# Performance work log

Hardware: AMD Instinct MI355X
Metric: run time of the kernel (lower is better)

## Reference

```python
import jax, jax.numpy as jnp
import numpy as np

B, C, H, W = 8, 256, 128, 128
KC, VC, HEADS = 256, 256, 8


def setup_inputs() -> dict:
    key = jax.random.key(0)
    ks = jax.random.split(key, 10)
    s = 0.05
    return {
        "x": jax.random.normal(ks[0], (B, C, H, W), jnp.float32),
        "Wk": jax.random.normal(ks[1], (KC, C), jnp.float32) * s,
        "bk": jax.random.normal(ks[2], (KC,), jnp.float32) * s,
        "Wq": jax.random.normal(ks[3], (KC, C), jnp.float32) * s,
        "bq": jax.random.normal(ks[4], (KC,), jnp.float32) * s,
        "Wv": jax.random.normal(ks[5], (VC, C), jnp.float32) * s,
        "bv": jax.random.normal(ks[6], (VC,), jnp.float32) * s,
        "Wr": jax.random.normal(ks[7], (C, VC), jnp.float32) * s,
        "br": jax.random.normal(ks[8], (C,), jnp.float32) * s,
        "head_count": HEADS,
    }


def reference(x, Wk, bk, Wq, bq, Wv, bv, Wr, br, head_count):
    n, c, h, w = x.shape
    hw = h * w
    xf = x.reshape(n, c, hw)  # [n, C, S]
    # 1x1 convs == per-pixel linear projections
    keys = jnp.einsum('kc,ncs->nks', Wk, xf) + bk[None, :, None]
    queries = jnp.einsum('kc,ncs->nks', Wq, xf) + bq[None, :, None]
    values = jnp.einsum('vc,ncs->nvs', Wv, xf) + bv[None, :, None]

    dk = Wk.shape[0] // head_count
    dv = Wv.shape[0] // head_count
    # split heads along channel dim (matches torch channel slicing)
    K = jax.nn.softmax(keys.reshape(n, head_count, dk, hw), axis=-1)   # softmax over spatial
    Q = jax.nn.softmax(queries.reshape(n, head_count, dk, hw), axis=2) # softmax over key dim
    V = values.reshape(n, head_count, dv, hw)

    # context = K @ V^T : [n, h, dk, dv]
    ctx = jnp.einsum('nhks,nhvs->nhkv', K, V)
    # attended = ctx^T @ Q : [n, h, dv, S]
    att = jnp.einsum('nhkv,nhks->nhvs', ctx, Q).reshape(n, head_count * dv, h, w)

    attention = jnp.einsum('ov,nvhw->nohw', Wr, att) + br[None, :, None, None]
    # attention map: per-head mean over key dim, then mean over heads
    attention_map = K.mean(axis=2).mean(axis=1).reshape(n, h, w)
    # torch returns the LAST head's context (loop variable after the loop)
    context_last = ctx[:, -1]
    return attention, context_last, attention_map
```

## Files before the change

### kernel.cpp

```cpp
#include <hip/hip_runtime.h>
#include <hip/hip_bf16.h>

typedef float f32x4 __attribute__((ext_vector_type(4)));
typedef short s16x8 __attribute__((ext_vector_type(8)));
typedef short s16x4 __attribute__((ext_vector_type(4)));
typedef __bf16 bf16x8 __attribute__((ext_vector_type(8)));
typedef unsigned short u16;

#define DEVI __device__ __forceinline__

static constexpr int    HW      = 16384;
static constexpr size_t BSTRIDE = (size_t)256 * HW;

static constexpr size_t oXBT   = 0;
static constexpr size_t oEK    = oXBT  + (size_t)8 * HW * 256 * 2;
static constexpr size_t oQT    = oEK   + (size_t)8 * 256 * HW * 2;
static constexpr size_t oVB    = oQT   + (size_t)8 * HW * 256 * 2;
static constexpr size_t oWK    = oVB   + (size_t)8 * 256 * HW * 2;
static constexpr size_t oBIAS  = oWK   + (size_t)768 * 256 * 2;
static constexpr size_t oISE   = oBIAS + 4096;
static constexpr size_t oPS    = oISE  + 8192;
static constexpr size_t oCTX   = oPS   + (size_t)256 * 2048 * 4;
static constexpr size_t oMB    = oCTX  + (size_t)64 * 1024 * 4;
static constexpr size_t oCPART = oMB   + (size_t)8 * 256 * 256 * 2;
static constexpr size_t oMPART = oCPART + (size_t)4096 * 1024 * 4;

DEVI float bf2f(short x) {
  unsigned u = ((unsigned)(unsigned short)x) << 16;
  return __builtin_bit_cast(float, u);
}
DEVI u16 f2bf(float x) { return __builtin_bit_cast(u16, (__bf16)x); }

DEVI void gld16(const void* g, void* l) {
  __builtin_amdgcn_global_load_lds(
      (__attribute__((address_space(1))) void*)(g),
      (__attribute__((address_space(3))) void*)(l), 16, 0, 0);
}

__global__ __launch_bounds__(256) void k_prep(
    const float* __restrict__ Wk, const float* __restrict__ Wq, const float* __restrict__ Wv,
    const float* __restrict__ bk, const float* __restrict__ bq, const float* __restrict__ bv,
    u16* __restrict__ Wkqv, float* __restrict__ bias)
{
  int i = blockIdx.x * 256 + threadIdx.x;
  for (int p = i; p < 768 * 256; p += 64 * 256) {
    float v = (p < 65536) ? Wk[p] : (p < 131072 ? Wq[p - 65536] : Wv[p - 131072]);
    Wkqv[p] = f2bf(v);
  }
  if (i < 768) bias[i] = (i < 256) ? bk[i] : (i < 512 ? bq[i - 256] : bv[i - 512]);
}

__global__ __launch_bounds__(256) void k_transpose(const float* __restrict__ in_, u16* __restrict__ out)
{
  __shared__ u16 lds[64 * 256];
  const int t = threadIdx.x;
  const int n = blockIdx.y;
  const int s0 = blockIdx.x * 64;
  const float* src = in_ + ((size_t)n * 256 + t) * HW + s0;
  #pragma unroll
  for (int i = 0; i < 16; ++i) {
    f32x4 v = *(const f32x4*)(src + i * 4);
    #pragma unroll
    for (int j = 0; j < 4; ++j) lds[(i * 4 + j) * 256 + t] = f2bf(v[j]);
  }
  __syncthreads();
  s16x8* gp = (s16x8*)(out + (size_t)n * BSTRIDE + (size_t)s0 * 256);
  const s16x8* lp = (const s16x8*)lds;
  #pragma unroll
  for (int i = 0; i < 8; ++i) gp[t + i * 256] = lp[t + i * 256];
}


#define GEMM_CORE(Ab, Bb)                                                                   \
  u16* Al = smem;                                                                           \
  u16* Bl = smem + 16384;                                                                   \
  auto STAGE = [&](int buf, int kt) {                                                       \
    const int k0 = kt * 64;                                                                 \
    _Pragma("unroll")                                                                       \
    for (int i = 0; i < 4; ++i) {                                                           \
      const int r_ = i * 32 + (t >> 3);                                                     \
      const int cs = (((t & 7) ^ (r_ & 7)) * 8);                                            \
      gld16((Ab) + (size_t)r_ * 256 + k0 + cs, Al + buf * 8192 + i * 2048 + t * 8);         \
      gld16((Bb) + (size_t)r_ * 256 + k0 + cs, Bl + buf * 8192 + i * 2048 + t * 8);         \
    }                                                                                       \
  };                                                                                        \
  f32x4 acc[4][4] = {};                                                                     \
  STAGE(0, 0); STAGE(1, 1);                                                                 \
  _Pragma("unroll")                                                                         \
  for (int kt = 0; kt < 4; ++kt) {                                                          \
    if (kt < 3) asm volatile("s_waitcnt vmcnt(8)" ::: "memory");                            \
    else        asm volatile("s_waitcnt vmcnt(0)" ::: "memory");                            \
    __builtin_amdgcn_s_barrier();                                                           \
    const int buf = kt & 1;                                                                 \
    _Pragma("unroll")                                                                       \
    for (int ks = 0; ks < 2; ++ks) {                                                        \
      bf16x8 af[4], bff[4];                                                                 \
      _Pragma("unroll")                                                                     \
      for (int g = 0; g < 4; ++g) {                                                         \
        const int mrow = wm + g * 16 + l15;                                                 \
        const int srow = wn + g * 16 + l15;                                                 \
        af[g]  = *(const bf16x8*)&Al[buf * 8192 + mrow * 64 + (((ks * 4 + l4) ^ (mrow & 7)) * 8)]; \
        bff[g] = *(const bf16x8*)&Bl[buf * 8192 + srow * 64 + (((ks * 4 + l4) ^ (srow & 7)) * 8)]; \
      }                                                                                     \
      __builtin_amdgcn_s_setprio(1);                                                        \
      _Pragma("unroll")                                                                     \
      for (int mg = 0; mg < 4; ++mg)                                                        \
        _Pragma("unroll")                                                                   \
        for (int ng = 0; ng < 4; ++ng)                                                      \
          acc[mg][ng] = __builtin_amdgcn_mfma_f32_16x16x32_bf16(af[mg], bff[ng], acc[mg][ng], 0, 0, 0); \
      __builtin_amdgcn_s_setprio(0);                                                        \
    }                                                                                       \
    asm volatile("s_waitcnt lgkmcnt(0)" ::: "memory");                                      \
    __builtin_amdgcn_s_barrier();                                                           \
    if (kt < 2) STAGE(buf, kt + 2);                                                         \
  }

__global__ __launch_bounds__(256, 2) void k_proj(
    const u16* __restrict__ W, const u16* __restrict__ xbT, const float* __restrict__ bias,
    u16* __restrict__ ek, u16* __restrict__ qT, u16* __restrict__ vb, float* __restrict__ ps)
{
  __shared__ u16 smem[32768];
  const int t = threadIdx.x;
  const int L = blockIdx.x;
  const int n  = L & 7;
  const int idx = L >> 3;
  const int mb = idx % 6;
  const int sb = idx / 6;
  const int m0 = mb * 128, s0 = sb * 128;
  const int lane = t & 63;
  const int l15 = lane & 15, l4 = (lane >> 4) & 3;
  const int wv = t >> 6;
  const int wm = (wv & 1) * 64, wn = (wv >> 1) * 64;
  const u16* Ab = W + (size_t)m0 * 256;
  const u16* Bb = xbT + (size_t)n * BSTRIDE + (size_t)s0 * 256;

  GEMM_CORE(Ab, Bb)

  #pragma unroll
  for (int mg = 0; mg < 4; ++mg)
    #pragma unroll
    for (int r = 0; r < 4; ++r) {
      const float bb = bias[m0 + wm + mg * 16 + l4 * 4 + r];
      #pragma unroll
      for (int ng = 0; ng < 4; ++ng) acc[mg][ng][r] += bb;
    }

  const int rowBase = (mb & 1) * 128;

  if (mb < 2) {
    #pragma unroll
    for (int mg = 0; mg < 4; ++mg)
      #pragma unroll
      for (int r = 0; r < 4; ++r) {
        float s_ = 0.f;
        #pragma unroll
        for (int ng = 0; ng < 4; ++ng) {
          const float e = __expf(acc[mg][ng][r]);
          acc[mg][ng][r] = e; s_ += e;
        }
        s_ += __shfl_xor(s_, 1); s_ += __shfl_xor(s_, 2);
        s_ += __shfl_xor(s_, 4); s_ += __shfl_xor(s_, 8);
        if (l15 == 0) {
          const int row = rowBase + wm + mg * 16 + l4 * 4 + r;
          ps[((size_t)(sb * 2 + (wn >> 6))) * 2048 + n * 256 + row] = s_;
        }
      }
    u16* O = ek + (size_t)n * BSTRIDE;
    #pragma unroll
    for (int mg = 0; mg < 4; ++mg)
      #pragma unroll
      for (int r = 0; r < 4; ++r) {
        const size_t row = rowBase + wm + mg * 16 + l4 * 4 + r;
        u16* op = O + row * HW + s0 + wn + l15;
        #pragma unroll
        for (int ng = 0; ng < 4; ++ng) op[ng * 16] = f2bf(acc[mg][ng][r]);
      }
  } else if (mb < 4) {
    #pragma unroll
    for (int hh = 0; hh < 2; ++hh)
      #pragma unroll
      for (int ng = 0; ng < 4; ++ng) {
        float s = 0.f;
        #pragma unroll
        for (int mg = hh * 2; mg < hh * 2 + 2; ++mg)
          #pragma unroll
          for (int r = 0; r < 4; ++r) { const float e = __expf(acc[mg][ng][r]); acc[mg][ng][r] = e; s += e; }
        s += __shfl_xor(s, 16);
        s += __shfl_xor(s, 32);
        const float inv = 1.f / s;
        #pragma unroll
        for (int mg = hh * 2; mg < hh * 2 + 2; ++mg)
          #pragma unroll
          for (int r = 0; r < 4; ++r) acc[mg][ng][r] *= inv;
      }
    __syncthreads();
    #pragma unroll
    for (int mg = 0; mg < 4; ++mg)
      #pragma unroll
      for (int ng = 0; ng < 4; ++ng)
        #pragma unroll
        for (int r = 0; r < 4; ++r) {
          const int srow = wn + ng * 16 + l15;
          const int mcol = wm + mg * 16 + l4 * 4 + r;
          smem[srow * 136 + mcol] = f2bf(acc[mg][ng][r]);
        }
    __syncthreads();
    u16* O = qT + (size_t)n * BSTRIDE + (size_t)s0 * 256 + rowBase;
    #pragma unroll
    for (int it = 0; it < 8; ++it) {
      const int row = it * 16 + (t >> 4);
      *(s16x8*)(O + (size_t)row * 256 + (t & 15) * 8) = *(const s16x8*)&smem[row * 136 + (t & 15) * 8];
    }
  } else {
    u16* O = vb + (size_t)n * BSTRIDE;
    #pragma unroll
    for (int mg = 0; mg < 4; ++mg)
      #pragma unroll
      for (int r = 0; r < 4; ++r) {
        const size_t row = rowBase + wm + mg * 16 + l4 * 4 + r;
        u16* op = O + row * HW + s0 + wn + l15;
        #pragma unroll
        for (int ng = 0; ng < 4; ++ng) op[ng * 16] = f2bf(acc[mg][ng][r]);
      }
  }
}

__global__ __launch_bounds__(256, 2) void k_attn(
    const u16* __restrict__ Mb, const u16* __restrict__ qT, const float* __restrict__ br,
    float* __restrict__ Out)
{
  __shared__ u16 smem[32768];
  const int t = threadIdx.x;
  const int L = blockIdx.x;
  const int n = L & 7;
  const int idx = L >> 3;
  const int m0 = (idx & 1) * 128;
  const int s0 = (idx >> 1) * 128;
  const int lane = t & 63;
  const int l15 = lane & 15, l4 = (lane >> 4) & 3;
  const int wv = t >> 6;
  const int wm = (wv & 1) * 64, wn = (wv >> 1) * 64;
  const u16* Ab = Mb + (size_t)n * 65536 + (size_t)m0 * 256;
  const u16* Bb = qT + (size_t)n * BSTRIDE + (size_t)s0 * 256;

  GEMM_CORE(Ab, Bb)

  float* O = Out + (size_t)n * BSTRIDE;
  #pragma unroll
  for (int mg = 0; mg < 4; ++mg)
    #pragma unroll
    for (int r = 0; r < 4; ++r) {
      const size_t row = m0 + wm + mg * 16 + l4 * 4 + r;
      const float bb = br[row];
      float* op = O + row * HW + s0 + wn + l15;
      #pragma unroll
      for (int ng = 0; ng < 4; ++ng) op[ng * 16] = acc[mg][ng][r] + bb;
    }
}

__global__ __launch_bounds__(256) void k_inv(const float* __restrict__ ps, float* __restrict__ ise)
{
  const int i = blockIdx.x * 256 + threadIdx.x;
  float s = 0.f;
  for (int b = 0; b < 256; ++b) s += ps[(size_t)b * 2048 + i];
  ise[i] = 1.f / s;
}

__global__ __launch_bounds__(64) void k_ctx_part(
    const u16* __restrict__ ek, const u16* __restrict__ vb, const float* __restrict__ ise,
    float* __restrict__ cpart, float* __restrict__ mpart)
{
  const int blk = blockIdx.x;
  const int chunk = blk & 63, nh = blk >> 6;
  const int h = nh & 7, n = nh >> 3;
  const int lane = threadIdx.x;
  const int l15 = lane & 15, l4 = lane >> 4;
  const u16* kb = ek + ((size_t)n * 256 + h * 32) * HW;
  const u16* vv = vb + ((size_t)n * 256 + h * 32) * HW;
  const float iv0 = ise[n * 256 + h * 32 + l15];
  const float iv1 = ise[n * 256 + h * 32 + 16 + l15];
  f32x4 acc[2][2] = {};
  float macc[8][8] = {};
  const int sbase = chunk * 256 + l4 * 8;
  #pragma unroll
  for (int ks = 0; ks < 8; ++ks) {
    const int sb = sbase + ks * 32;
    bf16x8 ef[2], vf[2];
    #pragma unroll
    for (int g = 0; g < 2; ++g) {
      ef[g] = *(const bf16x8*)(kb + (size_t)(g * 16 + l15) * HW + sb);
      vf[g] = *(const bf16x8*)(vv + (size_t)(g * 16 + l15) * HW + sb);
    }
    #pragma unroll
    for (int j = 0; j < 8; ++j)
      macc[ks][j] = fmaf(iv0, (float)ef[0][j], fmaf(iv1, (float)ef[1][j], macc[ks][j]));
    #pragma unroll
    for (int a = 0; a < 2; ++a)
      #pragma unroll
      for (int b = 0; b < 2; ++b)
        acc[a][b] = __builtin_amdgcn_mfma_f32_16x16x32_bf16(ef[a], vf[b], acc[a][b], 0, 0, 0);
  }
  float* op = cpart + (size_t)blk * 1024;
  #pragma unroll
  for (int a = 0; a < 2; ++a)
    #pragma unroll
    for (int b = 0; b < 2; ++b)
      #pragma unroll
      for (int r = 0; r < 4; ++r)
        op[(a * 16 + l4 * 4 + r) * 32 + b * 16 + l15] = acc[a][b][r];
  #pragma unroll
  for (int ks = 0; ks < 8; ++ks)
    #pragma unroll
    for (int j = 0; j < 8; ++j) {
      float v = macc[ks][j];
      v += __shfl_xor(v, 1); v += __shfl_xor(v, 2);
      v += __shfl_xor(v, 4); v += __shfl_xor(v, 8);
      macc[ks][j] = v;
    }
  if (l15 == 0) {
    float* mp = mpart + ((size_t)h * 8 + n) * HW + sbase;
    #pragma unroll
    for (int ks = 0; ks < 8; ++ks) {
      f32x4 a = {macc[ks][0], macc[ks][1], macc[ks][2], macc[ks][3]};
      f32x4 b = {macc[ks][4], macc[ks][5], macc[ks][6], macc[ks][7]};
      *(f32x4*)(mp + ks * 32)     = a;
      *(f32x4*)(mp + ks * 32 + 4) = b;
    }
  }
}

__global__ __launch_bounds__(256) void k_ctx_reduce(
    const float* __restrict__ cpart, const float* __restrict__ ise,
    float* __restrict__ ctx, float* __restrict__ dctx)
{
  const int nh = blockIdx.x, n = nh >> 3, h = nh & 7, t = threadIdx.x;
  f32x4 a = {};
  for (int c = 0; c < 64; ++c) a += *(const f32x4*)(cpart + ((size_t)nh * 64 + c) * 1024 + t * 4);
  const float inv = ise[n * 256 + h * 32 + (t >> 3)];
  a *= inv;
  *(f32x4*)(ctx + (size_t)nh * 1024 + t * 4) = a;
  if (h == 7) *(f32x4*)(dctx + (size_t)n * 1024 + t * 4) = a;
}

__global__ __launch_bounds__(256) void k_mmat(
    const float* __restrict__ ctx, const float* __restrict__ Wr, u16* __restrict__ Mb)
{
  const int nh = blockIdx.x, n = nh >> 3, h = nh & 7, o = threadIdx.x;
  __shared__ float cl[1024];
  #pragma unroll
  for (int i = 0; i < 4; ++i) cl[o + i * 256] = ctx[(size_t)nh * 1024 + o + i * 256];
  __syncthreads();
  float wr[32];
  const float* wp = Wr + (size_t)o * 256 + h * 32;
  #pragma unroll
  for (int v = 0; v < 32; ++v) wr[v] = wp[v];
  u16* mp = Mb + ((size_t)n * 256 + o) * 256 + h * 32;
  #pragma unroll 4
  for (int k = 0; k < 32; ++k) {
    float s = 0.f;
    #pragma unroll
    for (int v = 0; v < 32; ++v) s += wr[v] * cl[k * 32 + v];
    mp[k] = f2bf(s);
  }
}

__global__ __launch_bounds__(256) void k_map_reduce(const float* __restrict__ mpart, float* __restrict__ dmap)
{
  const int i = blockIdx.x * 256 + threadIdx.x;
  f32x4 a = {};
  #pragma unroll
  for (int h = 0; h < 8; ++h) a += *(const f32x4*)(mpart + (size_t)h * 131072 + (size_t)i * 4);
  a *= (1.0f / 256.0f);
  *(f32x4*)(dmap + (size_t)i * 4) = a;
}

extern "C" void kernel_launch(void* const* d_in, const int* in_sizes, int n_in,
                              void* d_out, int out_size, void* d_ws, size_t ws_size,
                              hipStream_t stream)
{
  (void)in_sizes; (void)n_in; (void)out_size; (void)ws_size;
  const float* x  = (const float*)d_in[0];
  const float* Wk = (const float*)d_in[1];
  const float* bk = (const float*)d_in[2];
  const float* Wq = (const float*)d_in[3];
  const float* bq = (const float*)d_in[4];
  const float* Wv = (const float*)d_in[5];
  const float* bv = (const float*)d_in[6];
  const float* Wr = (const float*)d_in[7];
  const float* br = (const float*)d_in[8];

  char* ws = (char*)d_ws;
  u16*   xbT  = (u16*)(ws + oXBT);
  u16*   ek   = (u16*)(ws + oEK);
  u16*   qT   = (u16*)(ws + oQT);
  u16*   vb   = (u16*)(ws + oVB);
  u16*   Wkqv = (u16*)(ws + oWK);
  float* bias = (float*)(ws + oBIAS);
  float* ise  = (float*)(ws + oISE);
  float* ps   = (float*)(ws + oPS);
  float* ctx  = (float*)(ws + oCTX);
  u16*   Mb   = (u16*)(ws + oMB);
  float* cpart= (float*)(ws + oCPART);
  float* mpart= (float*)(ws + oMPART);

  float* attn = (float*)d_out;
  float* dctx = (float*)d_out + 33554432;
  float* dmap = (float*)d_out + 33562624;

  k_prep<<<64, 256, 0, stream>>>(Wk, Wq, Wv, bk, bq, bv, Wkqv, bias);
  k_transpose<<<dim3(256, 8), 256, 0, stream>>>(x, xbT);
  k_proj<<<6144, 256, 0, stream>>>(Wkqv, xbT, bias, ek, qT, vb, ps);
  k_inv<<<8, 256, 0, stream>>>(ps, ise);
  k_ctx_part<<<4096, 64, 0, stream>>>(ek, vb, ise, cpart, mpart);
  k_ctx_reduce<<<64, 256, 0, stream>>>(cpart, ise, ctx, dctx);
  k_mmat<<<64, 256, 0, stream>>>(ctx, Wr, Mb);
  k_map_reduce<<<128, 256, 0, stream>>>(mpart, dmap);
  k_attn<<<2048, 256, 0, stream>>>(Mb, qT, br, attn);
}
```

Before: 287.1 us.

## Make K/V projection and output GEMM persistent over four spatial tiles with vectorized stores

Splits the fused projection into a K/V kernel and a separate Q kernel. The K/V kernel and the new output GEMM kernel each loop over four consecutive 128-wide spatial tiles inside one block, keeping the double-buffered LDS pipeline running across tiles with hand-tuned vmcnt waits. The MFMA operand order is swapped so each lane holds contiguous spatial outputs, which allows 4-wide vector stores instead of scalar strided stores. The aim is to cut block launch overhead, pipeline prologue and epilogue bubbles, and uncoalesced writes. The cost is fewer blocks, so less parallelism, and fragile manual waitcnt counts.

```diff
diff --git a/kernel.cpp b/kernel.cpp
--- a/kernel.cpp
+++ b/kernel.cpp
@@ -70,6 +70,217 @@
   for (int i = 0; i < 8; ++i) gp[t + i * 256] = lp[t + i * 256];
 }
 
+
+__global__ __launch_bounds__(256, 2) void k_projKV(
+    const u16* __restrict__ W, const u16* __restrict__ xbT, const float* __restrict__ bias,
+    u16* __restrict__ ek, u16* __restrict__ vb, float* __restrict__ ps)
+{
+  __shared__ u16 smem[32768];
+  const int t = threadIdx.x;
+  const int L = blockIdx.x;
+  const int n = L & 7;
+  const int idx = L >> 3;
+  const int mbi = idx & 3;
+  const int sq  = idx >> 2;
+  const bool isK = (mbi < 2);
+  const int m0 = (mbi & 1) * 128;
+  const int aBase = (isK ? 0 : 512) + m0;
+  const int lane = t & 63;
+  const int l15 = lane & 15, l4 = (lane >> 4) & 3;
+  const int wv = t >> 6;
+  const int wm = (wv & 1) * 64, wn = (wv >> 1) * 64;
+  const u16* Ab = W + (size_t)aBase * 256;
+  const u16* Bb = xbT + (size_t)n * BSTRIDE;
+  u16* Al = smem;
+  u16* Bl = smem + 16384;
+
+  float biasv[4];
+  #pragma unroll
+  for (int mf = 0; mf < 4; ++mf) biasv[mf] = bias[aBase + wm + mf * 16 + l15];
+
+  const int rr = t >> 3;
+  const int csh = t & 7;
+  auto STAGE = [&](int buf, int it) {
+    const int k0 = (it & 3) * 64;
+    const size_t s_t0 = (size_t)((sq * 4 + (it >> 2)) * 128);
+    #pragma unroll
+    for (int i = 0; i < 4; ++i) {
+      const int row = i * 32 + rr;
+      const int cs = (csh ^ (row & 7)) * 8;
+      gld16(Ab + (size_t)row * 256 + k0 + cs,          Al + buf * 8192 + i * 2048 + t * 8);
+      gld16(Bb + (s_t0 + row) * 256 + k0 + cs,         Bl + buf * 8192 + i * 2048 + t * 8);
+    }
+  };
+
+  f32x4 acc[4][4] = {};
+  STAGE(0, 0); STAGE(1, 1);
+
+  u16* outb = (isK ? ek : vb) + (size_t)n * BSTRIDE;
+
+  #pragma unroll
+  for (int it = 0; it < 16; ++it) {
+    if (it == 15)                          asm volatile("s_waitcnt vmcnt(0)" ::: "memory");
+    else if ((it & 3) <= 1 && it >= 4) {
+      if (isK) asm volatile("s_waitcnt vmcnt(28)" ::: "memory");
+      else     asm volatile("s_waitcnt vmcnt(24)" ::: "memory");
+    } else                                 asm volatile("s_waitcnt vmcnt(8)" ::: "memory");
+    __builtin_amdgcn_s_barrier();
+
+    const int buf = it & 1;
+    #pragma unroll
+    for (int ks = 0; ks < 2; ++ks) {
+      bf16x8 af[4], bff[4];
+      #pragma unroll
+      for (int g = 0; g < 4; ++g) {
+        const int mrow = wm + g * 16 + l15;
+        const int srow = wn + g * 16 + l15;
+        af[g]  = *(const bf16x8*)&Al[buf * 8192 + mrow * 64 + (((ks * 4 + l4) ^ (mrow & 7)) * 8)];
+        bff[g] = *(const bf16x8*)&Bl[buf * 8192 + srow * 64 + (((ks * 4 + l4) ^ (srow & 7)) * 8)];
+      }
+      __builtin_amdgcn_s_setprio(1);
+      #pragma unroll
+      for (int sf = 0; sf < 4; ++sf)
+        #pragma unroll
+        for (int mf = 0; mf < 4; ++mf)
+          acc[sf][mf] = __builtin_amdgcn_mfma_f32_16x16x32_bf16(bff[sf], af[mf], acc[sf][mf], 0, 0, 0);
+      __builtin_amdgcn_s_setprio(0);
+    }
+    asm volatile("s_waitcnt lgkmcnt(0)" ::: "memory");
+    __builtin_amdgcn_s_barrier();
+    if (it < 14) STAGE(buf, it + 2);
+
+    if ((it & 3) == 3) {
+      const int tile = it >> 2;
+      const int s0t = (sq * 4 + tile) * 128;
+      const int stile = sq * 4 + tile;
+      if (isK) {
+        float rs[4] = {0.f, 0.f, 0.f, 0.f};
+        #pragma unroll
+        for (int sf = 0; sf < 4; ++sf)
+          #pragma unroll
+          for (int mf = 0; mf < 4; ++mf) {
+            s16x4 pk;
+            #pragma unroll
+            for (int r = 0; r < 4; ++r) {
+              const float e = __expf(acc[sf][mf][r] + biasv[mf]);
+              rs[mf] += e;
+              pk[r] = (short)f2bf(e);
+            }
+            *(s16x4*)(outb + (size_t)(m0 + wm + mf * 16 + l15) * HW + s0t + wn + sf * 16 + l4 * 4) = pk;
+          }
+        #pragma unroll
+        for (int mf = 0; mf < 4; ++mf) {
+          float v = rs[mf];
+          v += __shfl_xor(v, 16); v += __shfl_xor(v, 32);
+          if (l4 == 0)
+            ps[((size_t)(stile * 2 + (wn >> 6))) * 2048 + n * 256 + m0 + wm + mf * 16 + l15] = v;
+        }
+      } else {
+        #pragma unroll
+        for (int sf = 0; sf < 4; ++sf)
+          #pragma unroll
+          for (int mf = 0; mf < 4; ++mf) {
+            s16x4 pk;
+            #pragma unroll
+            for (int r = 0; r < 4; ++r) pk[r] = (short)f2bf(acc[sf][mf][r] + biasv[mf]);
+            *(s16x4*)(outb + (size_t)(m0 + wm + mf * 16 + l15) * HW + s0t + wn + sf * 16 + l4 * 4) = pk;
+          }
+      }
+      #pragma unroll
+      for (int sf = 0; sf < 4; ++sf)
+        #pragma unroll
+        for (int mf = 0; mf < 4; ++mf) acc[sf][mf] = f32x4{0.f, 0.f, 0.f, 0.f};
+    }
+  }
+}
+
+__global__ __launch_bounds__(256, 2) void k_attn2(
+    const u16* __restrict__ Mb, const u16* __restrict__ qT, const float* __restrict__ br,
+    float* __restrict__ Out)
+{
+  __shared__ u16 smem[32768];
+  const int t = threadIdx.x;
+  const int L = blockIdx.x;
+  const int n = L & 7;
+  const int idx = L >> 3;
+  const int mb = idx & 1;
+  const int sq = idx >> 1;
+  const int m0 = mb * 128;
+  const int lane = t & 63;
+  const int l15 = lane & 15, l4 = (lane >> 4) & 3;
+  const int wv = t >> 6;
+  const int wm = (wv & 1) * 64, wn = (wv >> 1) * 64;
+  const u16* Ab = Mb + (size_t)n * 65536 + (size_t)m0 * 256;
+  const u16* Bb = qT + (size_t)n * BSTRIDE;
+  u16* Al = smem;
+  u16* Bl = smem + 16384;
+
+  float biasv[4];
+  #pragma unroll
+  for (int mf = 0; mf < 4; ++mf) biasv[mf] = br[m0 + wm + mf * 16 + l15];
+
+  const int rr = t >> 3;
+  const int csh = t & 7;
+  auto STAGE = [&](int buf, int it) {
+    const int k0 = (it & 3) * 64;
+    const size_t s_t0 = (size_t)((sq * 4 + (it >> 2)) * 128);
+    #pragma unroll
+    for (int i = 0; i < 4; ++i) {
+      const int row = i * 32 + rr;
+      const int cs = (csh ^ (row & 7)) * 8;
+      gld16(Ab + (size_t)row * 256 + k0 + cs,  Al + buf * 8192 + i * 2048 + t * 8);
+      gld16(Bb + (s_t0 + row) * 256 + k0 + cs, Bl + buf * 8192 + i * 2048 + t * 8);
+    }
+  };
+
+  f32x4 acc[4][4] = {};
+  STAGE(0, 0); STAGE(1, 1);
+
+  float* ob = Out + (size_t)n * BSTRIDE;
+
+  #pragma unroll
+  for (int it = 0; it < 16; ++it) {
+    if (it == 15)                          asm volatile("s_waitcnt vmcnt(0)" ::: "memory");
+    else if ((it & 3) <= 1 && it >= 4)     asm volatile("s_waitcnt vmcnt(24)" ::: "memory");
+    else                                   asm volatile("s_waitcnt vmcnt(8)" ::: "memory");
+    __builtin_amdgcn_s_barrier();
+
+    const int buf = it & 1;
+    #pragma unroll
+    for (int ks = 0; ks < 2; ++ks) {
+      bf16x8 af[4], bff[4];
+      #pragma unroll
+      for (int g = 0; g < 4; ++g) {
+        const int mrow = wm + g * 16 + l15;
+        const int srow = wn + g * 16 + l15;
+        af[g]  = *(const bf16x8*)&Al[buf * 8192 + mrow * 64 + (((ks * 4 + l4) ^ (mrow & 7)) * 8)];
+        bff[g] = *(const bf16x8*)&Bl[buf * 8192 + srow * 64 + (((ks * 4 + l4) ^ (srow & 7)) * 8)];
+      }
+      __builtin_amdgcn_s_setprio(1);
+      #pragma unroll
+      for (int sf = 0; sf < 4; ++sf)
+        #pragma unroll
+        for (int mf = 0; mf < 4; ++mf)
+          acc[sf][mf] = __builtin_amdgcn_mfma_f32_16x16x32_bf16(bff[sf], af[mf], acc[sf][mf], 0, 0, 0);
+      __builtin_amdgcn_s_setprio(0);
+    }
+    asm volatile("s_waitcnt lgkmcnt(0)" ::: "memory");
+    __builtin_amdgcn_s_barrier();
+    if (it < 14) STAGE(buf, it + 2);
+
+    if ((it & 3) == 3) {
+      const int s0t = (sq * 4 + (it >> 2)) * 128;
+      #pragma unroll
+      for (int sf = 0; sf < 4; ++sf)
+        #pragma unroll
+        for (int mf = 0; mf < 4; ++mf) {
+          f32x4 o = acc[sf][mf] + biasv[mf];
+          *(f32x4*)(ob + (size_t)(m0 + wm + mf * 16 + l15) * HW + s0t + wn + sf * 16 + l4 * 4) = o;
+          acc[sf][mf] = f32x4{0.f, 0.f, 0.f, 0.f};
+        }
+    }
+  }
+}
 
 #define GEMM_CORE(Ab, Bb)                                                                   \
   u16* Al = smem;                                                                           \
@@ -115,18 +326,18 @@
     if (kt < 2) STAGE(buf, kt + 2);                                                         \
   }
 
-__global__ __launch_bounds__(256, 2) void k_proj(
+__global__ __launch_bounds__(256, 2) void k_projQ(
     const u16* __restrict__ W, const u16* __restrict__ xbT, const float* __restrict__ bias,
-    u16* __restrict__ ek, u16* __restrict__ qT, u16* __restrict__ vb, float* __restrict__ ps)
+    u16* __restrict__ qT)
 {
   __shared__ u16 smem[32768];
   const int t = threadIdx.x;
   const int L = blockIdx.x;
   const int n  = L & 7;
   const int idx = L >> 3;
-  const int mb = idx % 6;
-  const int sb = idx / 6;
-  const int m0 = mb * 128, s0 = sb * 128;
+  const int mbq = idx & 1;
+  const int sb  = idx >> 1;
+  const int m0 = 256 + mbq * 128, s0 = sb * 128;
   const int lane = t & 63;
   const int l15 = lane & 15, l4 = (lane >> 4) & 3;
   const int wv = t >> 6;
@@ -145,117 +356,41 @@
       for (int ng = 0; ng < 4; ++ng) acc[mg][ng][r] += bb;
     }
 
-  const int rowBase = (mb & 1) * 128;
-
-  if (mb < 2) {
-    #pragma unroll
-    for (int mg = 0; mg < 4; ++mg)
+  #pragma unroll
+  for (int hh = 0; hh < 2; ++hh)
+    #pragma unroll
+    for (int ng = 0; ng < 4; ++ng) {
+      float s = 0.f;
+      #pragma unroll
+      for (int mg = hh * 2; mg < hh * 2 + 2; ++mg)
+        #pragma unroll
+        for (int r = 0; r < 4; ++r) { const float e = __expf(acc[mg][ng][r]); acc[mg][ng][r] = e; s += e; }
+      s += __shfl_xor(s, 16);
+      s += __shfl_xor(s, 32);
+      const float inv = 1.f / s;
+      #pragma unroll
+      for (int mg = hh * 2; mg < hh * 2 + 2; ++mg)
+        #pragma unroll
+        for (int r = 0; r < 4; ++r) acc[mg][ng][r] *= inv;
+    }
+  __syncthreads();
+  #pragma unroll
+  for (int mg = 0; mg < 4; ++mg)
+    #pragma unroll
+    for (int ng = 0; ng < 4; ++ng)
       #pragma unroll
       for (int r = 0; r < 4; ++r) {
-        float s_ = 0.f;
-        #pragma unroll
-        for (int ng = 0; ng < 4; ++ng) {
-          const float e = __expf(acc[mg][ng][r]);
-          acc[mg][ng][r] = e; s_ += e;
-        }
-        s_ += __shfl_xor(s_, 1); s_ += __shfl_xor(s_, 2);
-        s_ += __shfl_xor(s_, 4); s_ += __shfl_xor(s_, 8);
-        if (l15 == 0) {
-          const int row = rowBase + wm + mg * 16 + l4 * 4 + r;
-          ps[((size_t)(sb * 2 + (wn >> 6))) * 2048 + n * 256 + row] = s_;
-        }
+        const int srow = wn + ng * 16 + l15;
+        const int mcol = wm + mg * 16 + l4 * 4 + r;
+        smem[srow * 136 + mcol] = f2bf(acc[mg][ng][r]);
       }
-    u16* O = ek + (size_t)n * BSTRIDE;
-    #pragma unroll
-    for (int mg = 0; mg < 4; ++mg)
-      #pragma unroll
-      for (int r = 0; r < 4; ++r) {
-        const size_t row = rowBase + wm + mg * 16 + l4 * 4 + r;
-        u16* op = O + row * HW + s0 + wn + l15;
-        #pragma unroll
-        for (int ng = 0; ng < 4; ++ng) op[ng * 16] = f2bf(acc[mg][ng][r]);
-      }
-  } else if (mb < 4) {
-    #pragma unroll
-    for (int hh = 0; hh < 2; ++hh)
-      #pragma unroll
-      for (int ng = 0; ng < 4; ++ng) {
-        float s = 0.f;
-        #pragma unroll
-        for (int mg = hh * 2; mg < hh * 2 + 2; ++mg)
-          #pragma unroll
-          for (int r = 0; r < 4; ++r) { const float e = __expf(acc[mg][ng][r]); acc[mg][ng][r] = e; s += e; }
-        s += __shfl_xor(s, 16);
-        s += __shfl_xor(s, 32);
-        const float inv = 1.f / s;
-        #pragma unroll
-        for (int mg = hh * 2; mg < hh * 2 + 2; ++mg)
-          #pragma unroll
-          for (int r = 0; r < 4; ++r) acc[mg][ng][r] *= inv;
-      }
-    __syncthreads();
-    #pragma unroll
-    for (int mg = 0; mg < 4; ++mg)
-      #pragma unroll
-      for (int ng = 0; ng < 4; ++ng)
-        #pragma unroll
-        for (int r = 0; r < 4; ++r) {
-          const int srow = wn + ng * 16 + l15;
-          const int mcol = wm + mg * 16 + l4 * 4 + r;
-          smem[srow * 136 + mcol] = f2bf(acc[mg][ng][r]);
-        }
-    __syncthreads();
-    u16* O = qT + (size_t)n * BSTRIDE + (size_t)s0 * 256 + rowBase;
-    #pragma unroll
-    for (int it = 0; it < 8; ++it) {
-      const int row = it * 16 + (t >> 4);
-      *(s16x8*)(O + (size_t)row * 256 + (t & 15) * 8) = *(const s16x8*)&smem[row * 136 + (t & 15) * 8];
-    }
-  } else {
-    u16* O = vb + (size_t)n * BSTRIDE;
-    #pragma unroll
-    for (int mg = 0; mg < 4; ++mg)
-      #pragma unroll
-      for (int r = 0; r < 4; ++r) {
-        const size_t row = rowBase + wm + mg * 16 + l4 * 4 + r;
-        u16* op = O + row * HW + s0 + wn + l15;
-        #pragma unroll
-        for (int ng = 0; ng < 4; ++ng) op[ng * 16] = f2bf(acc[mg][ng][r]);
-      }
-  }
-}
-
-__global__ __launch_bounds__(256, 2) void k_attn(
-    const u16* __restrict__ Mb, const u16* __restrict__ qT, const float* __restrict__ br,
-    float* __restrict__ Out)
-{
-  __shared__ u16 smem[32768];
-  const int t = threadIdx.x;
-  const int L = blockIdx.x;
-  const int n = L & 7;
-  const int idx = L >> 3;
-  const int m0 = (idx & 1) * 128;
-  const int s0 = (idx >> 1) * 128;
-  const int lane = t & 63;
-  const int l15 = lane & 15, l4 = (lane >> 4) & 3;
-  const int wv = t >> 6;
-  const int wm = (wv & 1) * 64, wn = (wv >> 1) * 64;
-  const u16* Ab = Mb + (size_t)n * 65536 + (size_t)m0 * 256;
-  const u16* Bb = qT + (size_t)n * BSTRIDE + (size_t)s0 * 256;
-
-  GEMM_CORE(Ab, Bb)
-
-  float* O = Out + (size_t)n * BSTRIDE;
-  #pragma unroll
-  for (int mg = 0; mg < 4; ++mg)
-    #pragma unroll
-    for (int r = 0; r < 4; ++r) {
-      const size_t row = m0 + wm + mg * 16 + l4 * 4 + r;
-      const float bb = br[row];
-      float* op = O + row * HW + s0 + wn + l15;
-      #pragma unroll
-      for (int ng = 0; ng < 4; ++ng) op[ng * 16] = acc[mg][ng][r] + bb;
-    }
+  __syncthreads();
+  u16* O = qT + (size_t)n * BSTRIDE + (size_t)s0 * 256 + mbq * 128;
+  #pragma unroll
+  for (int it = 0; it < 8; ++it) {
+    const int row = it * 16 + (t >> 4);
+    *(s16x8*)(O + (size_t)row * 256 + (t & 15) * 8) = *(const s16x8*)&smem[row * 136 + (t & 15) * 8];
+  }
 }
 
 __global__ __launch_bounds__(256) void k_inv(const float* __restrict__ ps, float* __restrict__ ise)
@@ -409,11 +544,12 @@
 
   k_prep<<<64, 256, 0, stream>>>(Wk, Wq, Wv, bk, bq, bv, Wkqv, bias);
   k_transpose<<<dim3(256, 8), 256, 0, stream>>>(x, xbT);
-  k_proj<<<6144, 256, 0, stream>>>(Wkqv, xbT, bias, ek, qT, vb, ps);
+  k_projKV<<<1024, 256, 0, stream>>>(Wkqv, xbT, bias, ek, vb, ps);
   k_inv<<<8, 256, 0, stream>>>(ps, ise);
+  k_projQ<<<2048, 256, 0, stream>>>(Wkqv, xbT, bias, qT);
   k_ctx_part<<<4096, 64, 0, stream>>>(ek, vb, ise, cpart, mpart);
   k_ctx_reduce<<<64, 256, 0, stream>>>(cpart, ise, ctx, dctx);
   k_mmat<<<64, 256, 0, stream>>>(ctx, Wr, Mb);
   k_map_reduce<<<128, 256, 0, stream>>>(mpart, dmap);
-  k_attn<<<2048, 256, 0, stream>>>(Mb, qT, br, attn);
-}
+  k_attn2<<<512, 256, 0, stream>>>(Mb, qT, br, attn);
+}
```

Measured after the change: 289.7 us, median of 2. About the same (+0.9%).
